# Optimization experiments

Hardware: AMD Instinct MI355X
Metric: run time of the kernel (lower is better)

## Reference

```python
import jax, jax.numpy as jnp
import numpy as np

N_SRC = 100000
N_DST = 50000
N_EDGES = 800000
D = 128
D_OUT = 128


def setup_inputs() -> dict:
    key = jax.random.key(0)
    ks = jax.random.split(key, 8)
    H_src = jax.random.normal(ks[0], (N_SRC, D), dtype=jnp.float32)
    H_dst = jax.random.normal(ks[1], (N_DST, D), dtype=jnp.float32)
    HBar_src = jax.random.normal(ks[2], (N_SRC, D), dtype=jnp.float32)
    agg_HBar_dst = jax.random.normal(ks[3], (N_DST, D), dtype=jnp.float32)
    src_idx = jax.random.randint(ks[4], (N_EDGES,), 0, N_SRC, dtype=jnp.int64)
    dst_idx = jax.random.randint(ks[5], (N_EDGES,), 0, N_DST, dtype=jnp.int64)
    # Linear(in_feats*2, out_feats): store as [2D, D_OUT] for x @ W + b
    gain = float(np.sqrt(2.0))  # calculate_gain('relu')
    bound = gain * float(np.sqrt(6.0 / (2 * D + D_OUT)))  # xavier_uniform
    W = jax.random.uniform(ks[6], (2 * D, D_OUT), dtype=jnp.float32,
                           minval=-bound, maxval=bound)
    b = jnp.zeros((D_OUT,), dtype=jnp.float32)
    return {"H_src": H_src, "H_dst": H_dst, "HBar_src": HBar_src,
            "agg_HBar_dst": agg_HBar_dst, "W": W, "b": b,
            "src_idx": src_idx, "dst_idx": dst_idx}


def reference(H_src, H_dst, HBar_src, agg_HBar_dst, W, b, src_idx, dst_idx):
    # training path of SAGEConvWithCV: copy_u('hdelta') + mean over dst
    hdelta = H_src - HBar_src                      # [N_src, D]
    msgs = jnp.take(hdelta, src_idx, axis=0)       # [E, D] gather
    summed = jax.ops.segment_sum(msgs, dst_idx, num_segments=N_DST)  # [N_dst, D]
    deg = jax.ops.segment_sum(jnp.ones((src_idx.shape[0],), dtype=H_src.dtype),
                              dst_idx, num_segments=N_DST)           # [N_dst]
    hdelta_new = summed / jnp.maximum(deg, 1.0)[:, None]  # mean (0 for isolated)
    h_neigh = agg_HBar_dst + hdelta_new
    h = jnp.concatenate([H_dst, h_neigh], axis=1) @ W + b  # [N_dst, D_OUT]
    return jax.nn.relu(h)
```

## Files before the change

kernel.cpp:

```cpp
#include <hip/hip_runtime.h>
#include <hip/hip_bf16.h>
#include <cstdint>
#include <cstddef>

#define NSRC 100000
#define NDST 50000
#define DOUT 128
#define KK2 256
#define NBUCK 196
#define CHUNK 4096

typedef __attribute__((ext_vector_type(8))) short bf16x8;
typedef __attribute__((ext_vector_type(4))) float f32x4;
typedef __attribute__((ext_vector_type(2))) float f32x2;

static __device__ __forceinline__ unsigned short f2bf(float f) {
    union { float f; uint32_t u; } v; v.f = f;
    uint32_t u = v.u;
    uint32_t r = u + 0x7FFFu + ((u >> 16) & 1u);
    return (unsigned short)(r >> 16);
}

__global__ __launch_bounds__(256) void k_prep(const float* __restrict__ W,
                                              unsigned short* __restrict__ WT,
                                              int* __restrict__ bcnt,
                                              int* __restrict__ bcur2) {
    int i = blockIdx.x * 256 + threadIdx.x;
    if (i < DOUT * KK2) {
        int n = i >> 8;
        int k = i & 255;
        WT[i] = f2bf(W[k * DOUT + n]);
    }
    if (i < 256) { bcnt[i] = 0; bcur2[i] = 0; }
}

__global__ __launch_bounds__(256) void k_hd_binA1(const float4* __restrict__ a,
                                                  const float4* __restrict__ b,
                                                  uint32_t* __restrict__ o, int n4,
                                                  const int* __restrict__ dst,
                                                  int* __restrict__ bcnt,
                                                  int E, int nbe) {
    __shared__ int bh[NBUCK];
    int t = threadIdx.x;
    if ((int)blockIdx.x < nbe) {
        if (t < NBUCK) bh[t] = 0;
        __syncthreads();
        int base = blockIdx.x * CHUNK;
        for (int i = t; i < CHUNK; i += 256) {
            int e = base + i;
            if (e < E) atomicAdd(&bh[dst[e] >> 8], 1);
        }
        __syncthreads();
        if (t < NBUCK && bh[t]) atomicAdd(&bcnt[t], bh[t]);
    } else {
        int i = ((int)blockIdx.x - nbe) * 256 + t;
        if (i < n4) {
            float4 x = a[i], y = b[i];
            uint32_t p = __builtin_amdgcn_cvt_pk_fp8_f32(x.x - y.x, x.y - y.y, 0u, false);
            p = __builtin_amdgcn_cvt_pk_fp8_f32(x.z - y.z, x.w - y.w, p, true);
            o[i] = p;
        }
    }
}

__global__ __launch_bounds__(256) void k_binA2(const int* __restrict__ src,
                                               const int* __restrict__ dst,
                                               const int* __restrict__ bcnt,
                                               int* __restrict__ bcur2,
                                               uint32_t* __restrict__ pairs, int E) {
    __shared__ int bh[NBUCK], lcur[NBUCK];
    __shared__ int wsum[4], wex[4];
    int t = threadIdx.x;
    int lane = t & 63, w = t >> 6;

    if (t < NBUCK) bh[t] = 0;
    __syncthreads();
    int base = blockIdx.x * CHUNK;
    for (int i = t; i < CHUNK; i += 256) {
        int e = base + i;
        if (e < E) atomicAdd(&bh[dst[e] >> 8], 1);
    }

    int v = (t < NBUCK) ? bcnt[t] : 0;
    int x = v;
#pragma unroll
    for (int s = 1; s < 64; s <<= 1) { int tt = __shfl_up(x, s, 64); if (lane >= s) x += tt; }
    if (lane == 63) wsum[w] = x;
    __syncthreads();
    if (t == 0) {
        int run = 0;
#pragma unroll
        for (int k = 0; k < 4; ++k) { wex[k] = run; run += wsum[k]; }
    }
    __syncthreads();
    int ex = wex[w] + x - v;

    if (t < NBUCK) lcur[t] = bh[t] ? (ex + atomicAdd(&bcur2[t], bh[t])) : 0;
    __syncthreads();

    for (int i = t; i < CHUNK; i += 256) {
        int e = base + i;
        if (e < E) {
            int d = dst[e];
            int pos = atomicAdd(&lcur[d >> 8], 1);
            pairs[pos] = ((uint32_t)(d & 255) << 24) | (uint32_t)src[e];
        }
    }
}

__global__ __launch_bounds__(256) void k_binB(const uint32_t* __restrict__ pairs,
                                              const int* __restrict__ bcnt,
                                              int* __restrict__ off,
                                              int* __restrict__ idx, int E) {
    __shared__ int lcnt[256];
    __shared__ int lcur[256];
    __shared__ int wsum[4], wex[4];
    __shared__ int gbase_s;
    int b = blockIdx.x, t = threadIdx.x;
    int lane = t & 63, w = t >> 6;

    int v = (t < NBUCK) ? bcnt[t] : 0;
    int x = v;
#pragma unroll
    for (int s = 1; s < 64; s <<= 1) { int tt = __shfl_up(x, s, 64); if (lane >= s) x += tt; }
    if (lane == 63) wsum[w] = x;
    __syncthreads();
    if (t == 0) {
        int run = 0;
#pragma unroll
        for (int k = 0; k < 4; ++k) { wex[k] = run; run += wsum[k]; }
    }
    __syncthreads();
    if (t == b) gbase_s = wex[w] + x - v;
    lcnt[t] = 0;
    __syncthreads();
    int gbase = gbase_s;
    int cnt = bcnt[b];

    for (int i = t; i < cnt; i += 256)
        atomicAdd(&lcnt[pairs[gbase + i] >> 24], 1);
    __syncthreads();

    v = lcnt[t];
    x = v;
#pragma unroll
    for (int s = 1; s < 64; s <<= 1) { int tt = __shfl_up(x, s, 64); if (lane >= s) x += tt; }
    if (lane == 63) wsum[w] = x;
    __syncthreads();
    if (t == 0) {
        int run = 0;
#pragma unroll
        for (int k = 0; k < 4; ++k) { wex[k] = run; run += wsum[k]; }
    }
    __syncthreads();
    int ex = wex[w] + x - v;
    lcur[t] = ex;
    int d = b * 256 + t;
    if (d < NDST) off[d] = gbase + ex;
    if (b == 0 && t == 0) off[NDST] = E;
    __syncthreads();

    for (int i = t; i < cnt; i += 256) {
        uint32_t p = pairs[gbase + i];
        int pos = atomicAdd(&lcur[p >> 24], 1);
        idx[gbase + pos] = (int)(p & 0xFFFFFFu);
    }
}

__global__ __launch_bounds__(256) void k_gath(const uint32_t* __restrict__ hd8u,
                                              const float4* __restrict__ agg4,
                                              const int* __restrict__ off,
                                              const int* __restrict__ idx,
                                              ushort4* __restrict__ Xn, int n) {
    int r = blockIdx.x * 4 + (threadIdx.x >> 6);
    if (r >= n) return;
    int lane = threadIdx.x & 63;
    int li = lane & 31, half = lane >> 5;
    float a0 = 0.f, a1 = 0.f, a2 = 0.f, a3 = 0.f;
    int o0 = off[r], o1 = off[r + 1];
    for (int c = o0; c < o1; c += 64) {
        int m = o1 - c; if (m > 64) m = 64;
        int myi = (lane < m) ? idx[c + lane] : 0;
        for (int j = 0; j < m; j += 16) {
            int t0 = j + 0 + half,  t1 = j + 2 + half,  t2 = j + 4 + half,  t3 = j + 6 + half;
            int t4 = j + 8 + half,  t5 = j + 10 + half, t6 = j + 12 + half, t7 = j + 14 + half;
            int s0 = __shfl(myi, t0), s1 = __shfl(myi, t1);
            int s2 = __shfl(myi, t2), s3 = __shfl(myi, t3);
            int s4 = __shfl(myi, t4), s5 = __shfl(myi, t5);
            int s6 = __shfl(myi, t6), s7 = __shfl(myi, t7);
            uint32_t u0 = hd8u[(size_t)s0 * 32 + li];
            uint32_t u1 = hd8u[(size_t)s1 * 32 + li];
            uint32_t u2 = hd8u[(size_t)s2 * 32 + li];
            uint32_t u3 = hd8u[(size_t)s3 * 32 + li];
            uint32_t u4 = hd8u[(size_t)s4 * 32 + li];
            uint32_t u5 = hd8u[(size_t)s5 * 32 + li];
            uint32_t u6 = hd8u[(size_t)s6 * 32 + li];
            uint32_t u7 = hd8u[(size_t)s7 * 32 + li];
            if (t0 >= m) u0 = 0;  if (t1 >= m) u1 = 0;
            if (t2 >= m) u2 = 0;  if (t3 >= m) u3 = 0;
            if (t4 >= m) u4 = 0;  if (t5 >= m) u5 = 0;
            if (t6 >= m) u6 = 0;  if (t7 >= m) u7 = 0;
            f32x2 l0 = __builtin_amdgcn_cvt_pk_f32_fp8(u0, false);
            f32x2 h0 = __builtin_amdgcn_cvt_pk_f32_fp8(u0, true);
            f32x2 l1 = __builtin_amdgcn_cvt_pk_f32_fp8(u1, false);
            f32x2 h1 = __builtin_amdgcn_cvt_pk_f32_fp8(u1, true);
            f32x2 l2 = __builtin_amdgcn_cvt_pk_f32_fp8(u2, false);
            f32x2 h2 = __builtin_amdgcn_cvt_pk_f32_fp8(u2, true);
            f32x2 l3 = __builtin_amdgcn_cvt_pk_f32_fp8(u3, false);
            f32x2 h3 = __builtin_amdgcn_cvt_pk_f32_fp8(u3, true);
            f32x2 l4 = __builtin_amdgcn_cvt_pk_f32_fp8(u4, false);
            f32x2 h4 = __builtin_amdgcn_cvt_pk_f32_fp8(u4, true);
            f32x2 l5 = __builtin_amdgcn_cvt_pk_f32_fp8(u5, false);
            f32x2 h5 = __builtin_amdgcn_cvt_pk_f32_fp8(u5, true);
            f32x2 l6 = __builtin_amdgcn_cvt_pk_f32_fp8(u6, false);
            f32x2 h6 = __builtin_amdgcn_cvt_pk_f32_fp8(u6, true);
            f32x2 l7 = __builtin_amdgcn_cvt_pk_f32_fp8(u7, false);
            f32x2 h7 = __builtin_amdgcn_cvt_pk_f32_fp8(u7, true);
            a0 += l0[0] + l1[0] + l2[0] + l3[0] + l4[0] + l5[0] + l6[0] + l7[0];
            a1 += l0[1] + l1[1] + l2[1] + l3[1] + l4[1] + l5[1] + l6[1] + l7[1];
            a2 += h0[0] + h1[0] + h2[0] + h3[0] + h4[0] + h5[0] + h6[0] + h7[0];
            a3 += h0[1] + h1[1] + h2[1] + h3[1] + h4[1] + h5[1] + h6[1] + h7[1];
        }
    }
    a0 += __shfl_xor(a0, 32); a1 += __shfl_xor(a1, 32);
    a2 += __shfl_xor(a2, 32); a3 += __shfl_xor(a3, 32);
    if (half == 0) {
        float inv = 1.0f / fmaxf((float)(o1 - o0), 1.0f);
        float4 g = agg4[(size_t)r * 32 + li];
        ushort4 u;
        u.x = f2bf(g.x + a0 * inv); u.y = f2bf(g.y + a1 * inv);
        u.z = f2bf(g.z + a2 * inv); u.w = f2bf(g.w + a3 * inv);
        Xn[(size_t)r * 32 + li] = u;
    }
}

__global__ __launch_bounds__(256) void k_gemm(const float4* __restrict__ Hd4,
                                              const unsigned short* __restrict__ Xn,
                                              const unsigned short* __restrict__ WT,
                                              const float* __restrict__ bias,
                                              float* __restrict__ out) {
    __shared__ __align__(16) unsigned short xt[16][264];
    int r0 = blockIdx.x * 16;
    int t = threadIdx.x;

    {
#pragma unroll
        for (int p = 0; p < 2; ++p) {
            int f = t + p * 256;
            int row = f >> 5, c4 = f & 31;
            float4 v = Hd4[(size_t)(r0 + row) * 32 + c4];
            ushort4 u;
            u.x = f2bf(v.x); u.y = f2bf(v.y); u.z = f2bf(v.z); u.w = f2bf(v.w);
            *(ushort4*)&xt[row][c4 * 4] = u;
        }
        int row = t >> 4, col8 = (t & 15) * 8;
        bf16x8 xv = *reinterpret_cast<const bf16x8*>(Xn + (size_t)(r0 + row) * 128 + col8);
        *(bf16x8*)&xt[row][128 + col8] = xv;
    }
    __syncthreads();

    int w = t >> 6, lane = t & 63;
    int lr = lane & 15, lg = lane >> 4;
    const bf16x8* B0 = reinterpret_cast<const bf16x8*>(WT + (size_t)(w * 32 + lr) * KK2 + lg * 8);
    const bf16x8* B1 = reinterpret_cast<const bf16x8*>(WT + (size_t)(w * 32 + 16 + lr) * KK2 + lg * 8);

    f32x4 acc0 = {0.f, 0.f, 0.f, 0.f};
    f32x4 acc1 = {0.f, 0.f, 0.f, 0.f};
#pragma unroll
    for (int kk = 0; kk < 8; ++kk) {
        bf16x8 av = *reinterpret_cast<const bf16x8*>(&xt[lr][lg * 8 + kk * 32]);
        acc0 = __builtin_amdgcn_mfma_f32_16x16x32_bf16(av, B0[kk * 4], acc0, 0, 0, 0);
        acc1 = __builtin_amdgcn_mfma_f32_16x16x32_bf16(av, B1[kk * 4], acc1, 0, 0, 0);
    }

    int col0 = w * 32 + lr;
    int col1 = col0 + 16;
    float bi0 = bias[col0], bi1 = bias[col1];
    int rowb = r0 + lg * 4;
#pragma unroll
    for (int j = 0; j < 4; ++j) {
        float v0 = acc0[j] + bi0;
        float v1 = acc1[j] + bi1;
        out[(size_t)(rowb + j) * DOUT + col0] = v0 > 0.f ? v0 : 0.f;
        out[(size_t)(rowb + j) * DOUT + col1] = v1 > 0.f ? v1 : 0.f;
    }
}

extern "C" void kernel_launch(void* const* d_in, const int* in_sizes, int n_in,
                              void* d_out, int out_size, void* d_ws, size_t ws_size,
                              hipStream_t stream) {
    const float* H_src    = (const float*)d_in[0];
    const float* H_dst    = (const float*)d_in[1];
    const float* HBar_src = (const float*)d_in[2];
    const float* agg      = (const float*)d_in[3];
    const float* W        = (const float*)d_in[4];
    const float* bias     = (const float*)d_in[5];
    const int*   src      = (const int*)d_in[6];
    const int*   dst      = (const int*)d_in[7];
    float* out = (float*)d_out;
    const int E = in_sizes[6];

    char* ws = (char*)d_ws;
    int* bcnt            = (int*)ws;
    int* bcur2           = (int*)(ws + 1024);
    int* off             = (int*)(ws + 3072);
    uint32_t* pairs      = (uint32_t*)(ws + 203264);
    int* idx_sorted      = (int*)(ws + 3403264);
    unsigned short* WT   = (unsigned short*)(ws + 6603264);
    unsigned short* hd8  = (unsigned short*)(ws + 6668800);
    unsigned short* Xn   = (unsigned short*)(ws + 19468800);

    const int NBE = (E + CHUNK - 1) / CHUNK;
    int n4 = NSRC * 32;
    int nStream = (n4 + 255) / 256;

    k_prep<<<128, 256, 0, stream>>>(W, WT, bcnt, bcur2);

    k_hd_binA1<<<NBE + nStream, 256, 0, stream>>>(
        (const float4*)H_src, (const float4*)HBar_src, (uint32_t*)hd8, n4,
        dst, bcnt, E, NBE);

    k_binA2<<<NBE, 256, 0, stream>>>(src, dst, bcnt, bcur2, pairs, E);
    k_binB<<<NBUCK, 256, 0, stream>>>(pairs, bcnt, off, idx_sorted, E);

    k_gath<<<(NDST + 3) / 4, 256, 0, stream>>>(
        (const uint32_t*)hd8, (const float4*)agg, off, idx_sorted,
        (ushort4*)Xn, NDST);

    k_gemm<<<NDST / 16, 256, 0, stream>>>(
        (const float4*)H_dst, Xn, WT, bias, out);
}
```

Before: 113.1 us.

## Fold weight prep into histogram kernel, use per-block partial counts, widen gather loads

The weight transpose/convert work is merged into the first histogram+fp8 kernel, which removes one launch. Global atomic bucket counters are replaced by per-block partial histograms, and the binning kernels then compute deterministic prefix offsets by reading all partials. That removes the separate histogram recount in k_binA2 and the zero-init of the counters. The gather kernel now loads 8 fp8 values per lane (uint2) over 16-lane groups and writes 8 bf16 at once, giving wider memory accesses and more edges in flight. The cost is that every binning block loops over roughly 196 partial rows, and the gather does an extra shuffle reduction stage.

New measurement: 140.6 us. 1.24x slower.

```diff
diff --git a/kernel.cpp b/kernel.cpp
--- a/kernel.cpp
+++ b/kernel.cpp
@@ -21,39 +21,33 @@
     return (unsigned short)(r >> 16);
 }
 
-__global__ __launch_bounds__(256) void k_prep(const float* __restrict__ W,
+__global__ __launch_bounds__(256) void k_all1(const float4* __restrict__ a,
+                                              const float4* __restrict__ b,
+                                              uint32_t* __restrict__ o, int n4,
+                                              const int* __restrict__ dst,
+                                              int* __restrict__ part,
+                                              const float* __restrict__ W,
                                               unsigned short* __restrict__ WT,
-                                              int* __restrict__ bcnt,
-                                              int* __restrict__ bcur2) {
-    int i = blockIdx.x * 256 + threadIdx.x;
-    if (i < DOUT * KK2) {
-        int n = i >> 8;
-        int k = i & 255;
-        WT[i] = f2bf(W[k * DOUT + n]);
-    }
-    if (i < 256) { bcnt[i] = 0; bcur2[i] = 0; }
-}
-
-__global__ __launch_bounds__(256) void k_hd_binA1(const float4* __restrict__ a,
-                                                  const float4* __restrict__ b,
-                                                  uint32_t* __restrict__ o, int n4,
-                                                  const int* __restrict__ dst,
-                                                  int* __restrict__ bcnt,
-                                                  int E, int nbe) {
+                                              int E, int nbe) {
     __shared__ int bh[NBUCK];
     int t = threadIdx.x;
-    if ((int)blockIdx.x < nbe) {
+    int bid = blockIdx.x;
+    if (bid < nbe) {
         if (t < NBUCK) bh[t] = 0;
         __syncthreads();
-        int base = blockIdx.x * CHUNK;
+        int base = bid * CHUNK;
         for (int i = t; i < CHUNK; i += 256) {
             int e = base + i;
             if (e < E) atomicAdd(&bh[dst[e] >> 8], 1);
         }
         __syncthreads();
-        if (t < NBUCK && bh[t]) atomicAdd(&bcnt[t], bh[t]);
+        part[bid * 256 + t] = (t < NBUCK) ? bh[t] : 0;
+    } else if (bid < nbe + 128) {
+        int i = (bid - nbe) * 256 + t;
+        int n = i >> 8, k = i & 255;
+        WT[i] = f2bf(W[k * DOUT + n]);
     } else {
-        int i = ((int)blockIdx.x - nbe) * 256 + t;
+        int i = (bid - nbe - 128) * 256 + t;
         if (i < n4) {
             float4 x = a[i], y = b[i];
             uint32_t p = __builtin_amdgcn_cvt_pk_fp8_f32(x.x - y.x, x.y - y.y, 0u, false);
@@ -65,23 +59,21 @@
 
 __global__ __launch_bounds__(256) void k_binA2(const int* __restrict__ src,
                                                const int* __restrict__ dst,
-                                               const int* __restrict__ bcnt,
-                                               int* __restrict__ bcur2,
-                                               uint32_t* __restrict__ pairs, int E) {
-    __shared__ int bh[NBUCK], lcur[NBUCK];
+                                               const int* __restrict__ part,
+                                               uint32_t* __restrict__ pairs,
+                                               int E, int nbe) {
+    __shared__ int lcur[NBUCK];
     __shared__ int wsum[4], wex[4];
-    int t = threadIdx.x;
-    int lane = t & 63, w = t >> 6;
-
-    if (t < NBUCK) bh[t] = 0;
-    __syncthreads();
-    int base = blockIdx.x * CHUNK;
-    for (int i = t; i < CHUNK; i += 256) {
-        int e = base + i;
-        if (e < E) atomicAdd(&bh[dst[e] >> 8], 1);
-    }
-
-    int v = (t < NBUCK) ? bcnt[t] : 0;
+    int t = threadIdx.x, lane = t & 63, w = t >> 6;
+    int bid = blockIdx.x;
+
+    int tot = 0, pre = 0;
+    for (int j = 0; j < nbe; ++j) {
+        int p = part[j * 256 + t];
+        pre += (j < bid) ? p : 0;
+        tot += p;
+    }
+    int v = (t < NBUCK) ? tot : 0;
     int x = v;
 #pragma unroll
     for (int s = 1; s < 64; s <<= 1) { int tt = __shfl_up(x, s, 64); if (lane >= s) x += tt; }
@@ -94,10 +86,10 @@
     }
     __syncthreads();
     int ex = wex[w] + x - v;
-
-    if (t < NBUCK) lcur[t] = bh[t] ? (ex + atomicAdd(&bcur2[t], bh[t])) : 0;
-    __syncthreads();
-
+    if (t < NBUCK) lcur[t] = ex + pre;
+    __syncthreads();
+
+    int base = bid * CHUNK;
     for (int i = t; i < CHUNK; i += 256) {
         int e = base + i;
         if (e < E) {
@@ -109,17 +101,20 @@
 }
 
 __global__ __launch_bounds__(256) void k_binB(const uint32_t* __restrict__ pairs,
-                                              const int* __restrict__ bcnt,
+                                              const int* __restrict__ part,
                                               int* __restrict__ off,
-                                              int* __restrict__ idx, int E) {
+                                              int* __restrict__ idx,
+                                              int E, int nbe) {
     __shared__ int lcnt[256];
     __shared__ int lcur[256];
     __shared__ int wsum[4], wex[4];
-    __shared__ int gbase_s;
+    __shared__ int gbase_s, cnt_s;
     int b = blockIdx.x, t = threadIdx.x;
     int lane = t & 63, w = t >> 6;
 
-    int v = (t < NBUCK) ? bcnt[t] : 0;
+    int tot = 0;
+    for (int j = 0; j < nbe; ++j) tot += part[j * 256 + t];
+    int v = (t < NBUCK) ? tot : 0;
     int x = v;
 #pragma unroll
     for (int s = 1; s < 64; s <<= 1) { int tt = __shfl_up(x, s, 64); if (lane >= s) x += tt; }
@@ -131,11 +126,11 @@
         for (int k = 0; k < 4; ++k) { wex[k] = run; run += wsum[k]; }
     }
     __syncthreads();
-    if (t == b) gbase_s = wex[w] + x - v;
+    if (t == b) { gbase_s = wex[w] + x - v; cnt_s = tot; }
     lcnt[t] = 0;
     __syncthreads();
     int gbase = gbase_s;
-    int cnt = bcnt[b];
+    int cnt = cnt_s;
 
     for (int i = t; i < cnt; i += 256)
         atomicAdd(&lcnt[pairs[gbase + i] >> 24], 1);
@@ -167,70 +162,74 @@
     }
 }
 
-__global__ __launch_bounds__(256) void k_gath(const uint32_t* __restrict__ hd8u,
+__global__ __launch_bounds__(256) void k_gath(const uint2* __restrict__ hd2,
                                               const float4* __restrict__ agg4,
                                               const int* __restrict__ off,
                                               const int* __restrict__ idx,
-                                              ushort4* __restrict__ Xn, int n) {
+                                              bf16x8* __restrict__ Xn, int n) {
     int r = blockIdx.x * 4 + (threadIdx.x >> 6);
     if (r >= n) return;
     int lane = threadIdx.x & 63;
-    int li = lane & 31, half = lane >> 5;
+    int li = lane & 15, q = lane >> 4;
     float a0 = 0.f, a1 = 0.f, a2 = 0.f, a3 = 0.f;
+    float a4 = 0.f, a5 = 0.f, a6 = 0.f, a7 = 0.f;
     int o0 = off[r], o1 = off[r + 1];
     for (int c = o0; c < o1; c += 64) {
         int m = o1 - c; if (m > 64) m = 64;
         int myi = (lane < m) ? idx[c + lane] : 0;
-        for (int j = 0; j < m; j += 16) {
-            int t0 = j + 0 + half,  t1 = j + 2 + half,  t2 = j + 4 + half,  t3 = j + 6 + half;
-            int t4 = j + 8 + half,  t5 = j + 10 + half, t6 = j + 12 + half, t7 = j + 14 + half;
+        for (int j = 0; j < m; j += 32) {
+            int t0 = j + q,      t1 = j + 4 + q,  t2 = j + 8 + q,  t3 = j + 12 + q;
+            int t4 = j + 16 + q, t5 = j + 20 + q, t6 = j + 24 + q, t7 = j + 28 + q;
             int s0 = __shfl(myi, t0), s1 = __shfl(myi, t1);
             int s2 = __shfl(myi, t2), s3 = __shfl(myi, t3);
             int s4 = __shfl(myi, t4), s5 = __shfl(myi, t5);
             int s6 = __shfl(myi, t6), s7 = __shfl(myi, t7);
-            uint32_t u0 = hd8u[(size_t)s0 * 32 + li];
-            uint32_t u1 = hd8u[(size_t)s1 * 32 + li];
-            uint32_t u2 = hd8u[(size_t)s2 * 32 + li];
-            uint32_t u3 = hd8u[(size_t)s3 * 32 + li];
-            uint32_t u4 = hd8u[(size_t)s4 * 32 + li];
-            uint32_t u5 = hd8u[(size_t)s5 * 32 + li];
-            uint32_t u6 = hd8u[(size_t)s6 * 32 + li];
-            uint32_t u7 = hd8u[(size_t)s7 * 32 + li];
-            if (t0 >= m) u0 = 0;  if (t1 >= m) u1 = 0;
-            if (t2 >= m) u2 = 0;  if (t3 >= m) u3 = 0;
-            if (t4 >= m) u4 = 0;  if (t5 >= m) u5 = 0;
-            if (t6 >= m) u6 = 0;  if (t7 >= m) u7 = 0;
-            f32x2 l0 = __builtin_amdgcn_cvt_pk_f32_fp8(u0, false);
-            f32x2 h0 = __builtin_amdgcn_cvt_pk_f32_fp8(u0, true);
-            f32x2 l1 = __builtin_amdgcn_cvt_pk_f32_fp8(u1, false);
-            f32x2 h1 = __builtin_amdgcn_cvt_pk_f32_fp8(u1, true);
-            f32x2 l2 = __builtin_amdgcn_cvt_pk_f32_fp8(u2, false);
-            f32x2 h2 = __builtin_amdgcn_cvt_pk_f32_fp8(u2, true);
-            f32x2 l3 = __builtin_amdgcn_cvt_pk_f32_fp8(u3, false);
-            f32x2 h3 = __builtin_amdgcn_cvt_pk_f32_fp8(u3, true);
-            f32x2 l4 = __builtin_amdgcn_cvt_pk_f32_fp8(u4, false);
-            f32x2 h4 = __builtin_amdgcn_cvt_pk_f32_fp8(u4, true);
-            f32x2 l5 = __builtin_amdgcn_cvt_pk_f32_fp8(u5, false);
-            f32x2 h5 = __builtin_amdgcn_cvt_pk_f32_fp8(u5, true);
-            f32x2 l6 = __builtin_amdgcn_cvt_pk_f32_fp8(u6, false);
-            f32x2 h6 = __builtin_amdgcn_cvt_pk_f32_fp8(u6, true);
-            f32x2 l7 = __builtin_amdgcn_cvt_pk_f32_fp8(u7, false);
-            f32x2 h7 = __builtin_amdgcn_cvt_pk_f32_fp8(u7, true);
-            a0 += l0[0] + l1[0] + l2[0] + l3[0] + l4[0] + l5[0] + l6[0] + l7[0];
-            a1 += l0[1] + l1[1] + l2[1] + l3[1] + l4[1] + l5[1] + l6[1] + l7[1];
-            a2 += h0[0] + h1[0] + h2[0] + h3[0] + h4[0] + h5[0] + h6[0] + h7[0];
-            a3 += h0[1] + h1[1] + h2[1] + h3[1] + h4[1] + h5[1] + h6[1] + h7[1];
-        }
-    }
+            uint2 u0 = hd2[(size_t)s0 * 16 + li];
+            uint2 u1 = hd2[(size_t)s1 * 16 + li];
+            uint2 u2 = hd2[(size_t)s2 * 16 + li];
+            uint2 u3 = hd2[(size_t)s3 * 16 + li];
+            uint2 u4 = hd2[(size_t)s4 * 16 + li];
+            uint2 u5 = hd2[(size_t)s5 * 16 + li];
+            uint2 u6 = hd2[(size_t)s6 * 16 + li];
+            uint2 u7 = hd2[(size_t)s7 * 16 + li];
+            if (t0 >= m) { u0.x = 0; u0.y = 0; }
+            if (t1 >= m) { u1.x = 0; u1.y = 0; }
+            if (t2 >= m) { u2.x = 0; u2.y = 0; }
+            if (t3 >= m) { u3.x = 0; u3.y = 0; }
+            if (t4 >= m) { u4.x = 0; u4.y = 0; }
+            if (t5 >= m) { u5.x = 0; u5.y = 0; }
+            if (t6 >= m) { u6.x = 0; u6.y = 0; }
+            if (t7 >= m) { u7.x = 0; u7.y = 0; }
+#define ACC8(U) { \
+            f32x2 lo0 = __builtin_amdgcn_cvt_pk_f32_fp8(U.x, false); \
+            f32x2 hi0 = __builtin_amdgcn_cvt_pk_f32_fp8(U.x, true);  \
+            f32x2 lo1 = __builtin_amdgcn_cvt_pk_f32_fp8(U.y, false); \
+            f32x2 hi1 = __builtin_amdgcn_cvt_pk_f32_fp8(U.y, true);  \
+            a0 += lo0[0]; a1 += lo0[1]; a2 += hi0[0]; a3 += hi0[1];  \
+            a4 += lo1[0]; a5 += lo1[1]; a6 += hi1[0]; a7 += hi1[1];  }
+            ACC8(u0) ACC8(u1) ACC8(u2) ACC8(u3)
+            ACC8(u4) ACC8(u5) ACC8(u6) ACC8(u7)
+#undef ACC8
+        }
+    }
+    a0 += __shfl_xor(a0, 16); a1 += __shfl_xor(a1, 16);
+    a2 += __shfl_xor(a2, 16); a3 += __shfl_xor(a3, 16);
+    a4 += __shfl_xor(a4, 16); a5 += __shfl_xor(a5, 16);
+    a6 += __shfl_xor(a6, 16); a7 += __shfl_xor(a7, 16);
     a0 += __shfl_xor(a0, 32); a1 += __shfl_xor(a1, 32);
     a2 += __shfl_xor(a2, 32); a3 += __shfl_xor(a3, 32);
-    if (half == 0) {
+    a4 += __shfl_xor(a4, 32); a5 += __shfl_xor(a5, 32);
+    a6 += __shfl_xor(a6, 32); a7 += __shfl_xor(a7, 32);
+    if (q == 0) {
         float inv = 1.0f / fmaxf((float)(o1 - o0), 1.0f);
-        float4 g = agg4[(size_t)r * 32 + li];
-        ushort4 u;
-        u.x = f2bf(g.x + a0 * inv); u.y = f2bf(g.y + a1 * inv);
-        u.z = f2bf(g.z + a2 * inv); u.w = f2bf(g.w + a3 * inv);
-        Xn[(size_t)r * 32 + li] = u;
+        float4 g0 = agg4[(size_t)r * 32 + li * 2];
+        float4 g1 = agg4[(size_t)r * 32 + li * 2 + 1];
+        bf16x8 u;
+        u[0] = (short)f2bf(g0.x + a0 * inv); u[1] = (short)f2bf(g0.y + a1 * inv);
+        u[2] = (short)f2bf(g0.z + a2 * inv); u[3] = (short)f2bf(g0.w + a3 * inv);
+        u[4] = (short)f2bf(g1.x + a4 * inv); u[5] = (short)f2bf(g1.y + a5 * inv);
+        u[6] = (short)f2bf(g1.z + a6 * inv); u[7] = (short)f2bf(g1.w + a7 * inv);
+        Xn[(size_t)r * 16 + li] = u;
     }
 }
 
@@ -301,31 +300,28 @@
     const int E = in_sizes[6];
 
     char* ws = (char*)d_ws;
-    int* bcnt            = (int*)ws;
-    int* bcur2           = (int*)(ws + 1024);
-    int* off             = (int*)(ws + 3072);
-    uint32_t* pairs      = (uint32_t*)(ws + 203264);
-    int* idx_sorted      = (int*)(ws + 3403264);
-    unsigned short* WT   = (unsigned short*)(ws + 6603264);
-    unsigned short* hd8  = (unsigned short*)(ws + 6668800);
-    unsigned short* Xn   = (unsigned short*)(ws + 19468800);
+    int* part            = (int*)ws;
+    int* off             = (int*)(ws + 200704);
+    uint32_t* pairs      = (uint32_t*)(ws + 401408);
+    int* idx_sorted      = (int*)(ws + 3601408);
+    unsigned short* WT   = (unsigned short*)(ws + 6801408);
+    unsigned short* hd8  = (unsigned short*)(ws + 6866944);
+    unsigned short* Xn   = (unsigned short*)(ws + 19666944);
 
     const int NBE = (E + CHUNK - 1) / CHUNK;
     int n4 = NSRC * 32;
     int nStream = (n4 + 255) / 256;
 
-    k_prep<<<128, 256, 0, stream>>>(W, WT, bcnt, bcur2);
-
-    k_hd_binA1<<<NBE + nStream, 256, 0, stream>>>(
+    k_all1<<<NBE + 128 + nStream, 256, 0, stream>>>(
         (const float4*)H_src, (const float4*)HBar_src, (uint32_t*)hd8, n4,
-        dst, bcnt, E, NBE);
-
-    k_binA2<<<NBE, 256, 0, stream>>>(src, dst, bcnt, bcur2, pairs, E);
-    k_binB<<<NBUCK, 256, 0, stream>>>(pairs, bcnt, off, idx_sorted, E);
+        dst, part, W, WT, E, NBE);
+
+    k_binA2<<<NBE, 256, 0, stream>>>(src, dst, part, pairs, E, NBE);
+    k_binB<<<NBUCK, 256, 0, stream>>>(pairs, part, off, idx_sorted, E, NBE);
 
     k_gath<<<(NDST + 3) / 4, 256, 0, stream>>>(
-        (const uint32_t*)hd8, (const float4*)agg, off, idx_sorted,
-        (ushort4*)Xn, NDST);
+        (const uint2*)hd8, (const float4*)agg, off, idx_sorted,
+        (bf16x8*)Xn, NDST);
 
     k_gemm<<<NDST / 16, 256, 0, stream>>>(
         (const float4*)H_dst, Xn, WT, bias, out);
```
